# Kernel tuning notes

Hardware: AMD Instinct MI355X
Metric: run time of the kernel (lower is better)

The kernel has to match this reference:

```python
import jax, jax.numpy as jnp
import numpy as np

N = 500000   # num_nodes
B = 512      # batch_size
D = 128      # node_dim
G = 128      # global_dim
MC = 64      # max_cubes
M = 24       # max_moves_per_cube
H = 128      # MLP hidden
NEG = -1000000000.0


def setup_inputs() -> dict:
    key = jax.random.key(0)
    ks = jax.random.split(key, 8)
    node_features = jax.random.normal(ks[0], (N, D), jnp.float32)
    global_features = jax.random.normal(ks[1], (B, G), jnp.float32)
    cube_mask = jax.random.randint(ks[2], (N,), 0, 2) == 1
    batch = jnp.sort(jax.random.randint(ks[3], (N,), 0, B))
    move_mask = jax.random.randint(ks[4], (B, MC, M), 0, 2) == 1
    W1 = jax.random.normal(ks[5], (D + G, H), jnp.float32) * 0.05
    b1 = jnp.zeros((H,), jnp.float32)
    W2 = jax.random.normal(ks[6], (H, M), jnp.float32) * 0.05
    b2 = jnp.zeros((M,), jnp.float32)
    return {"node_features": node_features, "global_features": global_features,
            "W1": W1, "b1": b1, "W2": W2, "b2": b2,
            "cube_mask": cube_mask, "batch": batch, "move_mask": move_mask}


def reference(node_features, global_features, W1, b1, W2, b2, cube_mask, batch, move_mask):
    bsz = global_features.shape[0]
    max_cubes, moves = move_mask.shape[1], move_mask.shape[2]
    batch = batch.astype(jnp.int32)

    # gather global features per node, concat, small MLP (scores computed for all
    # nodes; only cube-node rows are ever scattered, matching the original math)
    combined = jnp.concatenate([node_features, global_features[batch]], axis=-1)  # [N, D+G]
    h = jax.nn.relu(combined @ W1 + b1)                                           # [N, H]
    scores = h @ W2 + b2                                                          # [N, M]

    # per-batch cumulative cube count (batch is sorted): cube_idx_in_batch
    mask_i = cube_mask.astype(jnp.int32)
    cum = jnp.cumsum(mask_i)                                   # inclusive prefix count of cubes
    counts = jax.ops.segment_sum(mask_i, batch, num_segments=bsz)
    offsets = jnp.concatenate([jnp.zeros((1,), jnp.int32),
                               jnp.cumsum(counts)[:-1].astype(jnp.int32)])
    cube_idx = cum - 1 - offsets[batch]                        # index of cube within its graph

    valid = cube_mask & (cube_idx < max_cubes)
    ib = jnp.where(valid, batch, bsz)      # out-of-range rows -> dropped
    ic = jnp.where(valid, cube_idx, 0)

    logits = jnp.full((bsz, max_cubes, moves), NEG, dtype=scores.dtype)
    logits = logits.at[ib, ic].set(scores, mode="drop")        # unique (ib, ic) per valid node

    logits_flat = logits.reshape(bsz, -1)
    logits_flat = jnp.where(move_mask.reshape(bsz, -1), logits_flat, NEG)
    return logits_flat
```

## Files before the change

kernel.cpp:

```cpp
#include <hip/hip_runtime.h>

typedef short bf16x8 __attribute__((ext_vector_type(8)));
typedef float f32x4 __attribute__((ext_vector_type(4)));

#define NEGV -1000000000.0f

__device__ __forceinline__ unsigned short f2bf(float f) {
    unsigned int u = __float_as_uint(f);
    u += 0x7FFFu + ((u >> 16) & 1u);
    return (unsigned short)(u >> 16);
}

__global__ void prep_kernel(const float* __restrict__ W1, const float* __restrict__ W2,
                            const int* __restrict__ batch, int N, int B,
                            int* __restrict__ batch_start,
                            unsigned short* __restrict__ w1t, unsigned short* __restrict__ w2t) {
    int idx = blockIdx.x * 256 + threadIdx.x;
    if (idx < N) {
        int bcur = batch[idx];
        if (idx == 0) {
            for (int bb = 0; bb <= bcur; ++bb) batch_start[bb] = 0;
        } else {
            int bprev = batch[idx - 1];
            for (int bb = bprev + 1; bb <= bcur; ++bb) batch_start[bb] = idx;
        }
        if (idx == N - 1) {
            for (int bb = bcur + 1; bb <= B; ++bb) batch_start[bb] = N;
        }
    }
    if (idx < 128 * 256) {
        int col = idx >> 8, k = idx & 255;
        w1t[col * 256 + k] = f2bf(W1[k * 128 + col]);
    }
    if (idx < 32 * 128) {
        int col = idx >> 7, k = idx & 127;
        w2t[col * 128 + k] = (col < 24) ? f2bf(W2[k * 24 + col]) : (unsigned short)0;
    }
}

__global__ void __launch_bounds__(256, 3)
fused_kernel(const float* __restrict__ nf, const float* __restrict__ gf,
             const unsigned short* __restrict__ w1t, const unsigned short* __restrict__ w2t,
             const float* __restrict__ b1, const float* __restrict__ b2,
             const int* __restrict__ cube_mask, const int* __restrict__ batch_start,
             const int* __restrict__ move_mask, float* __restrict__ out) {
    __shared__ __align__(16) char smemAB[(64 * 72 + 128 * 72) * 2];
    __shared__ __align__(16) unsigned short ldsW2[32][136];
    __shared__ int lds_node[64];
    __shared__ int wt[4];
    unsigned short (*ldsA)[72]  = (unsigned short (*)[72])smemAB;
    unsigned short (*ldsB)[72]  = (unsigned short (*)[72])(smemAB + 64 * 72 * 2);
    unsigned short (*ldsH)[136] = (unsigned short (*)[136])smemAB;

    int t = threadIdx.x;
    int blk = blockIdx.x;
    int lane = t & 63, w = t >> 6;

    int segs = batch_start[blk], sege = batch_start[blk + 1];

    if (t < 64) lds_node[t] = -1;

    {
        int col = t >> 3;
        int k0 = (t & 7) * 16;
        const unsigned short* src = w2t + col * 128 + k0;
        *(bf16x8*)&ldsW2[col][k0]     = *(const bf16x8*)(src);
        *(bf16x8*)&ldsW2[col][k0 + 8] = *(const bf16x8*)(src + 8);
    }
    int bcol = t >> 1, bh0 = (t & 1) * 32;
    bf16x8 fB[4];
    {
        const unsigned short* srcB = w1t + bcol * 256 + bh0;
        fB[0] = *(const bf16x8*)(srcB);      fB[1] = *(const bf16x8*)(srcB + 8);
        fB[2] = *(const bf16x8*)(srcB + 16); fB[3] = *(const bf16x8*)(srcB + 24);
    }
    int wm = w >> 1, wn = w & 1;
    float b1v[4];
#pragma unroll
    for (int nt = 0; nt < 4; ++nt) b1v[nt] = b1[wn * 64 + nt * 16 + (lane & 15)];
    float b2v[2];
    int mmv[8];
#pragma unroll
    for (int ct = 0; ct < 2; ++ct) {
        int m = ct * 16 + (lane & 15);
        if (m < 24) {
            b2v[ct] = b2[m];
#pragma unroll
            for (int rr = 0; rr < 4; ++rr) {
                int row = w * 16 + (lane >> 4) * 4 + rr;
                mmv[ct * 4 + rr] = move_mask[(size_t)(blk * 64 + row) * 24 + m];
            }
        } else {
            b2v[ct] = 0.f;
#pragma unroll
            for (int rr = 0; rr < 4; ++rr) mmv[ct * 4 + rr] = 0;
        }
    }
    __syncthreads();

    int found = 0;
    for (int pos = segs; pos < sege && found < 64; pos += 256) {
        int i = pos + t;
        int m = (i < sege) ? cube_mask[i] : 0;
        unsigned long long bal = __ballot(m != 0);
        int below = __popcll(bal & ((1ULL << lane) - 1ULL));
        if (lane == 0) wt[w] = __popcll(bal);
        __syncthreads();
        int waveOfs = 0, total = 0;
#pragma unroll
        for (int j = 0; j < 4; ++j) { int c = wt[j]; if (j < w) waveOfs += c; total += c; }
        int rank = found + waveOfs + below;
        if (m && rank < 64) lds_node[rank] = i;
        found += total;
        __syncthreads();
    }

    int r = t >> 2;
    int q = t & 3;
    int n = lds_node[r];
    int nrow = (n >= 0) ? n : 0;

    const float* srcN = nf + (size_t)nrow * 128 + q * 16;
    float4 fN[8];
#pragma unroll
    for (int i = 0; i < 4; ++i) {
        fN[i]     = *(const float4*)(srcN + i * 4);
        fN[4 + i] = *(const float4*)(srcN + 64 + i * 4);
    }

    f32x4 acc[2][4];
#pragma unroll
    for (int i = 0; i < 2; ++i)
#pragma unroll
        for (int j = 0; j < 4; ++j) acc[i][j] = (f32x4){0.f, 0.f, 0.f, 0.f};

    float4 fA[4];

#pragma unroll
    for (int c = 0; c < 4; ++c) {
        {
            float4 s0 = (c == 0) ? fN[0] : (c == 1) ? fN[4] : fA[0];
            float4 s1 = (c == 0) ? fN[1] : (c == 1) ? fN[5] : fA[1];
            float4 s2 = (c == 0) ? fN[2] : (c == 1) ? fN[6] : fA[2];
            float4 s3 = (c == 0) ? fN[3] : (c == 1) ? fN[7] : fA[3];
            unsigned short tmp[16];
            tmp[0]  = f2bf(s0.x); tmp[1]  = f2bf(s0.y); tmp[2]  = f2bf(s0.z); tmp[3]  = f2bf(s0.w);
            tmp[4]  = f2bf(s1.x); tmp[5]  = f2bf(s1.y); tmp[6]  = f2bf(s1.z); tmp[7]  = f2bf(s1.w);
            tmp[8]  = f2bf(s2.x); tmp[9]  = f2bf(s2.y); tmp[10] = f2bf(s2.z); tmp[11] = f2bf(s2.w);
            tmp[12] = f2bf(s3.x); tmp[13] = f2bf(s3.y); tmp[14] = f2bf(s3.z); tmp[15] = f2bf(s3.w);
            *(bf16x8*)&ldsA[r][q * 16]     = *(bf16x8*)&tmp[0];
            *(bf16x8*)&ldsA[r][q * 16 + 8] = *(bf16x8*)&tmp[8];
            *(bf16x8*)&ldsB[bcol][bh0]      = fB[0];
            *(bf16x8*)&ldsB[bcol][bh0 + 8]  = fB[1];
            *(bf16x8*)&ldsB[bcol][bh0 + 16] = fB[2];
            *(bf16x8*)&ldsB[bcol][bh0 + 24] = fB[3];
        }
        __syncthreads();
        if (c < 3) {
            const unsigned short* srcB = w1t + bcol * 256 + (c + 1) * 64 + bh0;
            fB[0] = *(const bf16x8*)(srcB);      fB[1] = *(const bf16x8*)(srcB + 8);
            fB[2] = *(const bf16x8*)(srcB + 16); fB[3] = *(const bf16x8*)(srcB + 24);
        }
        if (c == 1 || c == 2) {
            const float* srcG = gf + (size_t)blk * 128 + (c - 1) * 64 + q * 16;
            fA[0] = *(const float4*)(srcG);     fA[1] = *(const float4*)(srcG + 4);
            fA[2] = *(const float4*)(srcG + 8); fA[3] = *(const float4*)(srcG + 12);
        }
#pragma unroll
        for (int ks = 0; ks < 2; ++ks) {
            int ko = ks * 32 + (lane >> 4) * 8;
            bf16x8 af[2], bfr[4];
#pragma unroll
            for (int mt = 0; mt < 2; ++mt)
                af[mt] = *(const bf16x8*)&ldsA[wm * 32 + mt * 16 + (lane & 15)][ko];
#pragma unroll
            for (int nt = 0; nt < 4; ++nt)
                bfr[nt] = *(const bf16x8*)&ldsB[wn * 64 + nt * 16 + (lane & 15)][ko];
#pragma unroll
            for (int mt = 0; mt < 2; ++mt)
#pragma unroll
                for (int nt = 0; nt < 4; ++nt)
                    acc[mt][nt] = __builtin_amdgcn_mfma_f32_16x16x32_bf16(
                        af[mt], bfr[nt], acc[mt][nt], 0, 0, 0);
        }
        __syncthreads();
    }

#pragma unroll
    for (int nt = 0; nt < 4; ++nt) {
        int col = wn * 64 + nt * 16 + (lane & 15);
        float bias = b1v[nt];
#pragma unroll
        for (int mt = 0; mt < 2; ++mt) {
            int row0 = wm * 32 + mt * 16 + (lane >> 4) * 4;
#pragma unroll
            for (int rr = 0; rr < 4; ++rr) {
                float v = acc[mt][nt][rr] + bias;
                v = v > 0.f ? v : 0.f;
                ldsH[row0 + rr][col] = f2bf(v);
            }
        }
    }
    __syncthreads();

    f32x4 acc2[2];
    acc2[0] = (f32x4){0.f, 0.f, 0.f, 0.f};
    acc2[1] = (f32x4){0.f, 0.f, 0.f, 0.f};
#pragma unroll
    for (int ks = 0; ks < 4; ++ks) {
        int ko = ks * 32 + (lane >> 4) * 8;
        bf16x8 a2 = *(const bf16x8*)&ldsH[w * 16 + (lane & 15)][ko];
#pragma unroll
        for (int ct = 0; ct < 2; ++ct) {
            bf16x8 bw = *(const bf16x8*)&ldsW2[ct * 16 + (lane & 15)][ko];
            acc2[ct] = __builtin_amdgcn_mfma_f32_16x16x32_bf16(a2, bw, acc2[ct], 0, 0, 0);
        }
    }

#pragma unroll
    for (int ct = 0; ct < 2; ++ct) {
        int m = ct * 16 + (lane & 15);
        if (m >= 24) continue;
#pragma unroll
        for (int rr = 0; rr < 4; ++rr) {
            int row = w * 16 + (lane >> 4) * 4 + rr;
            size_t oidx = (size_t)(blk * 64 + row) * 24 + m;
            float v = acc2[ct][rr] + b2v[ct];
            bool keep = (lds_node[row] >= 0) && (mmv[ct * 4 + rr] != 0);
            out[oidx] = keep ? v : NEGV;
        }
    }
}

extern "C" void kernel_launch(void* const* d_in, const int* in_sizes, int n_in,
                              void* d_out, int out_size, void* d_ws, size_t ws_size,
                              hipStream_t stream) {
    const float* nf = (const float*)d_in[0];
    const float* gf = (const float*)d_in[1];
    const float* W1 = (const float*)d_in[2];
    const float* b1 = (const float*)d_in[3];
    const float* W2 = (const float*)d_in[4];
    const float* b2 = (const float*)d_in[5];
    const int* cube_mask = (const int*)d_in[6];
    const int* batch     = (const int*)d_in[7];
    const int* move_mask = (const int*)d_in[8];
    float* out = (float*)d_out;

    int N = in_sizes[6];
    int B = in_sizes[1] / 128;

    char* ws = (char*)d_ws;
    int* batch_start = (int*)(ws);
    unsigned short* w1t = (unsigned short*)(ws + 4096);
    unsigned short* w2t = (unsigned short*)(ws + 69632);

    int NB = (N + 255) / 256;
    prep_kernel<<<NB, 256, 0, stream>>>(W1, W2, batch, N, B, batch_start, w1t, w2t);
    fused_kernel<<<B, 256, 0, stream>>>(nf, gf, w1t, w2t, b1, b2,
                                        cube_mask, batch_start, move_mask, out);
    (void)n_in; (void)out_size; (void)ws_size;
}
```

Before: 17.86 us.

## Remove prep kernel; binary-search segments and convert W1/W2 in-block

Drops the separate prep kernel. Each block now finds its batch segment bounds by a 128-way parallel search over the sorted batch array, and converts W1/W2 from fp32 to bf16 into LDS itself. The GEMM chunk order is changed so the global-feature chunks run first while the search and node-feature loads are still in flight. This removes one launch and the 500k-element boundary pass, at the cost of every block redundantly reading and converting the fp32 weights and doing extra synchronised search rounds.

```diff
diff --git a/kernel.cpp b/kernel.cpp
--- a/kernel.cpp
+++ b/kernel.cpp
@@ -10,44 +10,22 @@
     u += 0x7FFFu + ((u >> 16) & 1u);
     return (unsigned short)(u >> 16);
 }
-
-__global__ void prep_kernel(const float* __restrict__ W1, const float* __restrict__ W2,
-                            const int* __restrict__ batch, int N, int B,
-                            int* __restrict__ batch_start,
-                            unsigned short* __restrict__ w1t, unsigned short* __restrict__ w2t) {
-    int idx = blockIdx.x * 256 + threadIdx.x;
-    if (idx < N) {
-        int bcur = batch[idx];
-        if (idx == 0) {
-            for (int bb = 0; bb <= bcur; ++bb) batch_start[bb] = 0;
-        } else {
-            int bprev = batch[idx - 1];
-            for (int bb = bprev + 1; bb <= bcur; ++bb) batch_start[bb] = idx;
-        }
-        if (idx == N - 1) {
-            for (int bb = bcur + 1; bb <= B; ++bb) batch_start[bb] = N;
-        }
-    }
-    if (idx < 128 * 256) {
-        int col = idx >> 8, k = idx & 255;
-        w1t[col * 256 + k] = f2bf(W1[k * 128 + col]);
-    }
-    if (idx < 32 * 128) {
-        int col = idx >> 7, k = idx & 127;
-        w2t[col * 128 + k] = (col < 24) ? f2bf(W2[k * 24 + col]) : (unsigned short)0;
-    }
+__device__ __forceinline__ unsigned int pack2(float a, float b) {
+    return (unsigned int)f2bf(a) | ((unsigned int)f2bf(b) << 16);
 }
 
 __global__ void __launch_bounds__(256, 3)
 fused_kernel(const float* __restrict__ nf, const float* __restrict__ gf,
-             const unsigned short* __restrict__ w1t, const unsigned short* __restrict__ w2t,
-             const float* __restrict__ b1, const float* __restrict__ b2,
-             const int* __restrict__ cube_mask, const int* __restrict__ batch_start,
-             const int* __restrict__ move_mask, float* __restrict__ out) {
+             const float* __restrict__ W1, const float* __restrict__ b1,
+             const float* __restrict__ W2, const float* __restrict__ b2,
+             const int* __restrict__ cube_mask, const int* __restrict__ batch,
+             const int* __restrict__ move_mask, float* __restrict__ out, int N) {
     __shared__ __align__(16) char smemAB[(64 * 72 + 128 * 72) * 2];
     __shared__ __align__(16) unsigned short ldsW2[32][136];
     __shared__ int lds_node[64];
     __shared__ int wt[4];
+    __shared__ unsigned long long swt[4];
+    __shared__ int seg[2];
     unsigned short (*ldsA)[72]  = (unsigned short (*)[72])smemAB;
     unsigned short (*ldsB)[72]  = (unsigned short (*)[72])(smemAB + 64 * 72 * 2);
     unsigned short (*ldsH)[136] = (unsigned short (*)[136])smemAB;
@@ -56,24 +34,14 @@
     int blk = blockIdx.x;
     int lane = t & 63, w = t >> 6;
 
-    int segs = batch_start[blk], sege = batch_start[blk + 1];
-
     if (t < 64) lds_node[t] = -1;
 
-    {
-        int col = t >> 3;
-        int k0 = (t & 7) * 16;
-        const unsigned short* src = w2t + col * 128 + k0;
-        *(bf16x8*)&ldsW2[col][k0]     = *(const bf16x8*)(src);
-        *(bf16x8*)&ldsW2[col][k0 + 8] = *(const bf16x8*)(src + 8);
-    }
-    int bcol = t >> 1, bh0 = (t & 1) * 32;
-    bf16x8 fB[4];
-    {
-        const unsigned short* srcB = w1t + bcol * 256 + bh0;
-        fB[0] = *(const bf16x8*)(srcB);      fB[1] = *(const bf16x8*)(srcB + 8);
-        fB[2] = *(const bf16x8*)(srcB + 16); fB[3] = *(const bf16x8*)(srcB + 24);
-    }
+    int w2col = t >> 3, w2k0 = (t & 7) * 16;
+    float w2v[16];
+#pragma unroll
+    for (int j = 0; j < 16; ++j)
+        w2v[j] = (w2col < 24) ? W2[(size_t)(w2k0 + j) * 24 + w2col] : 0.f;
+
     int wm = w >> 1, wn = w & 1;
     float b1v[4];
 #pragma unroll
@@ -96,7 +64,67 @@
             for (int rr = 0; rr < 4; ++rr) mmv[ct * 4 + rr] = 0;
         }
     }
-    __syncthreads();
+
+    int kp = t >> 3, hblk = t & 7;
+    float4 fW[8];
+    {
+        const float* s0 = W1 + (size_t)(128 + kp * 2) * 128 + hblk * 16;
+#pragma unroll
+        for (int i = 0; i < 4; ++i) {
+            fW[i]     = *(const float4*)(s0 + i * 4);
+            fW[4 + i] = *(const float4*)(s0 + 128 + i * 4);
+        }
+    }
+
+    int half = t >> 7, l = t & 127;
+    int target = blk + half;
+    int lo = -1, hi = N;
+#pragma unroll
+    for (int round = 0; round < 3; ++round) {
+        int span = hi - lo;
+        int pos = lo + (int)(((long long)span * (l + 1)) / 129);
+        int v = (pos >= 0) ? batch[pos] : -1;
+        unsigned long long bal = __ballot(v >= target);
+        if (lane == 0) swt[w] = bal;
+        __syncthreads();
+        unsigned long long mlow = swt[half * 2], mhigh = swt[half * 2 + 1];
+        int j0 = mlow ? __builtin_ctzll(mlow) : (mhigh ? 64 + __builtin_ctzll(mhigh) : -1);
+        if (j0 < 0) {
+            lo = lo + (int)(((long long)span * 128) / 129);
+        } else {
+            hi = lo + (int)(((long long)span * (j0 + 1)) / 129);
+            if (j0 > 0) lo = lo + (int)(((long long)span * j0) / 129);
+        }
+        __syncthreads();
+    }
+    if (l == 0) seg[half] = hi;
+
+#pragma unroll
+    for (int j = 0; j < 8; ++j)
+        *(unsigned int*)&ldsW2[w2col][w2k0 + 2 * j] = pack2(w2v[2 * j], w2v[2 * j + 1]);
+#pragma unroll
+    for (int j = 0; j < 16; ++j) {
+        float a  = ((const float*)&fW[j >> 2])[j & 3];
+        float bq = ((const float*)&fW[4 + (j >> 2)])[j & 3];
+        *(unsigned int*)&ldsB[hblk * 16 + j][kp * 2] = pack2(a, bq);
+    }
+    {
+        const float* s0 = W1 + (size_t)(192 + kp * 2) * 128 + hblk * 16;
+#pragma unroll
+        for (int i = 0; i < 4; ++i) {
+            fW[i]     = *(const float4*)(s0 + i * 4);
+            fW[4 + i] = *(const float4*)(s0 + 128 + i * 4);
+        }
+    }
+    int r = t >> 2, q = t & 3;
+    float4 fG[4];
+    {
+        const float* srcG = gf + (size_t)blk * 128 + q * 16;
+#pragma unroll
+        for (int i = 0; i < 4; ++i) fG[i] = *(const float4*)(srcG + i * 4);
+    }
+    __syncthreads();
+    int segs = seg[0], sege = seg[1];
 
     int found = 0;
     for (int pos = segs; pos < sege && found < 64; pos += 256) {
@@ -115,11 +143,8 @@
         __syncthreads();
     }
 
-    int r = t >> 2;
-    int q = t & 3;
     int n = lds_node[r];
     int nrow = (n >= 0) ? n : 0;
-
     const float* srcN = nf + (size_t)nrow * 128 + q * 16;
     float4 fN[8];
 #pragma unroll
@@ -134,57 +159,88 @@
 #pragma unroll
         for (int j = 0; j < 4; ++j) acc[i][j] = (f32x4){0.f, 0.f, 0.f, 0.f};
 
-    float4 fA[4];
-
-#pragma unroll
-    for (int c = 0; c < 4; ++c) {
-        {
-            float4 s0 = (c == 0) ? fN[0] : (c == 1) ? fN[4] : fA[0];
-            float4 s1 = (c == 0) ? fN[1] : (c == 1) ? fN[5] : fA[1];
-            float4 s2 = (c == 0) ? fN[2] : (c == 1) ? fN[6] : fA[2];
-            float4 s3 = (c == 0) ? fN[3] : (c == 1) ? fN[7] : fA[3];
-            unsigned short tmp[16];
-            tmp[0]  = f2bf(s0.x); tmp[1]  = f2bf(s0.y); tmp[2]  = f2bf(s0.z); tmp[3]  = f2bf(s0.w);
-            tmp[4]  = f2bf(s1.x); tmp[5]  = f2bf(s1.y); tmp[6]  = f2bf(s1.z); tmp[7]  = f2bf(s1.w);
-            tmp[8]  = f2bf(s2.x); tmp[9]  = f2bf(s2.y); tmp[10] = f2bf(s2.z); tmp[11] = f2bf(s2.w);
-            tmp[12] = f2bf(s3.x); tmp[13] = f2bf(s3.y); tmp[14] = f2bf(s3.z); tmp[15] = f2bf(s3.w);
-            *(bf16x8*)&ldsA[r][q * 16]     = *(bf16x8*)&tmp[0];
-            *(bf16x8*)&ldsA[r][q * 16 + 8] = *(bf16x8*)&tmp[8];
-            *(bf16x8*)&ldsB[bcol][bh0]      = fB[0];
-            *(bf16x8*)&ldsB[bcol][bh0 + 8]  = fB[1];
-            *(bf16x8*)&ldsB[bcol][bh0 + 16] = fB[2];
-            *(bf16x8*)&ldsB[bcol][bh0 + 24] = fB[3];
-        }
-        __syncthreads();
-        if (c < 3) {
-            const unsigned short* srcB = w1t + bcol * 256 + (c + 1) * 64 + bh0;
-            fB[0] = *(const bf16x8*)(srcB);      fB[1] = *(const bf16x8*)(srcB + 8);
-            fB[2] = *(const bf16x8*)(srcB + 16); fB[3] = *(const bf16x8*)(srcB + 24);
-        }
-        if (c == 1 || c == 2) {
-            const float* srcG = gf + (size_t)blk * 128 + (c - 1) * 64 + q * 16;
-            fA[0] = *(const float4*)(srcG);     fA[1] = *(const float4*)(srcG + 4);
-            fA[2] = *(const float4*)(srcG + 8); fA[3] = *(const float4*)(srcG + 12);
-        }
-#pragma unroll
-        for (int ks = 0; ks < 2; ++ks) {
-            int ko = ks * 32 + (lane >> 4) * 8;
-            bf16x8 af[2], bfr[4];
-#pragma unroll
-            for (int mt = 0; mt < 2; ++mt)
-                af[mt] = *(const bf16x8*)&ldsA[wm * 32 + mt * 16 + (lane & 15)][ko];
-#pragma unroll
-            for (int nt = 0; nt < 4; ++nt)
-                bfr[nt] = *(const bf16x8*)&ldsB[wn * 64 + nt * 16 + (lane & 15)][ko];
-#pragma unroll
-            for (int mt = 0; mt < 2; ++mt)
-#pragma unroll
-                for (int nt = 0; nt < 4; ++nt)
-                    acc[mt][nt] = __builtin_amdgcn_mfma_f32_16x16x32_bf16(
-                        af[mt], bfr[nt], acc[mt][nt], 0, 0, 0);
-        }
-        __syncthreads();
-    }
+#define STAGE_A(s0, s1, s2, s3) do {                                             \
+        unsigned short tmp[16];                                                  \
+        tmp[0]  = f2bf((s0).x); tmp[1]  = f2bf((s0).y); tmp[2]  = f2bf((s0).z); tmp[3]  = f2bf((s0).w); \
+        tmp[4]  = f2bf((s1).x); tmp[5]  = f2bf((s1).y); tmp[6]  = f2bf((s1).z); tmp[7]  = f2bf((s1).w); \
+        tmp[8]  = f2bf((s2).x); tmp[9]  = f2bf((s2).y); tmp[10] = f2bf((s2).z); tmp[11] = f2bf((s2).w); \
+        tmp[12] = f2bf((s3).x); tmp[13] = f2bf((s3).y); tmp[14] = f2bf((s3).z); tmp[15] = f2bf((s3).w); \
+        *(bf16x8*)&ldsA[r][q * 16]     = *(bf16x8*)&tmp[0];                      \
+        *(bf16x8*)&ldsA[r][q * 16 + 8] = *(bf16x8*)&tmp[8];                      \
+    } while (0)
+
+#define STAGE_B() do {                                                           \
+        _Pragma("unroll")                                                        \
+        for (int j = 0; j < 16; ++j) {                                           \
+            float a_  = ((const float*)&fW[j >> 2])[j & 3];                      \
+            float b_  = ((const float*)&fW[4 + (j >> 2)])[j & 3];                \
+            *(unsigned int*)&ldsB[hblk * 16 + j][kp * 2] = pack2(a_, b_);        \
+        }                                                                        \
+    } while (0)
+
+#define LOAD_W1(ch) do {                                                         \
+        const float* s0_ = W1 + (size_t)((ch) * 64 + kp * 2) * 128 + hblk * 16;  \
+        _Pragma("unroll")                                                        \
+        for (int i = 0; i < 4; ++i) {                                            \
+            fW[i]     = *(const float4*)(s0_ + i * 4);                           \
+            fW[4 + i] = *(const float4*)(s0_ + 128 + i * 4);                     \
+        }                                                                        \
+    } while (0)
+
+#define MFMA_CHUNK() do {                                                        \
+        _Pragma("unroll")                                                        \
+        for (int ks = 0; ks < 2; ++ks) {                                         \
+            int ko = ks * 32 + (lane >> 4) * 8;                                  \
+            bf16x8 af[2], bfr[4];                                                \
+            _Pragma("unroll")                                                    \
+            for (int mt = 0; mt < 2; ++mt)                                       \
+                af[mt] = *(const bf16x8*)&ldsA[wm * 32 + mt * 16 + (lane & 15)][ko]; \
+            _Pragma("unroll")                                                    \
+            for (int nt = 0; nt < 4; ++nt)                                       \
+                bfr[nt] = *(const bf16x8*)&ldsB[wn * 64 + nt * 16 + (lane & 15)][ko]; \
+            _Pragma("unroll")                                                    \
+            for (int mt = 0; mt < 2; ++mt)                                       \
+                _Pragma("unroll")                                                \
+                for (int nt = 0; nt < 4; ++nt)                                   \
+                    acc[mt][nt] = __builtin_amdgcn_mfma_f32_16x16x32_bf16(       \
+                        af[mt], bfr[nt], acc[mt][nt], 0, 0, 0);                  \
+        }                                                                        \
+    } while (0)
+
+    STAGE_A(fG[0], fG[1], fG[2], fG[3]);
+    __syncthreads();
+    {
+        const float* srcG = gf + (size_t)blk * 128 + 64 + q * 16;
+#pragma unroll
+        for (int i = 0; i < 4; ++i) fG[i] = *(const float4*)(srcG + i * 4);
+    }
+    MFMA_CHUNK();
+    __syncthreads();
+
+    STAGE_B();
+    LOAD_W1(0);
+    STAGE_A(fG[0], fG[1], fG[2], fG[3]);
+    __syncthreads();
+    MFMA_CHUNK();
+    __syncthreads();
+
+    STAGE_B();
+    LOAD_W1(1);
+    STAGE_A(fN[0], fN[1], fN[2], fN[3]);
+    __syncthreads();
+    MFMA_CHUNK();
+    __syncthreads();
+
+    STAGE_B();
+    STAGE_A(fN[4], fN[5], fN[6], fN[7]);
+    __syncthreads();
+    MFMA_CHUNK();
+    __syncthreads();
+
+#undef STAGE_A
+#undef STAGE_B
+#undef LOAD_W1
+#undef MFMA_CHUNK
 
 #pragma unroll
     for (int nt = 0; nt < 4; ++nt) {
@@ -249,14 +305,7 @@
     int N = in_sizes[6];
     int B = in_sizes[1] / 128;
 
-    char* ws = (char*)d_ws;
-    int* batch_start = (int*)(ws);
-    unsigned short* w1t = (unsigned short*)(ws + 4096);
-    unsigned short* w2t = (unsigned short*)(ws + 69632);
-
-    int NB = (N + 255) / 256;
-    prep_kernel<<<NB, 256, 0, stream>>>(W1, W2, batch, N, B, batch_start, w1t, w2t);
-    fused_kernel<<<B, 256, 0, stream>>>(nf, gf, w1t, w2t, b1, b2,
-                                        cube_mask, batch_start, move_mask, out);
-    (void)n_in; (void)out_size; (void)ws_size;
+    fused_kernel<<<B, 256, 0, stream>>>(nf, gf, W1, b1, W2, b2,
+                                        cube_mask, batch, move_mask, out, N);
+    (void)n_in; (void)out_size; (void)d_ws; (void)ws_size;
 }
```

Result: slower. 20.16 us (+12.9%).

## Overlap cube search with global-feature GEMM chunks using double-buffered LDS

Applied to the files above, without the earlier changes.

Reorders the first-layer GEMM so the two global-feature K-chunks are computed first, while the cube-mask scan and node-row gather are still in flight. The scan now reads a 1024-element window with one vectorised int4 load and a shuffle prefix sum, and only falls back to the ballot loop when that window does not hold 64 cubes. A and B tiles are double-buffered in LDS to remove one barrier per chunk. This doubles LDS use and lowers launch bounds to 2 blocks per CU, so fewer blocks can be resident.

```diff
diff --git a/kernel.cpp b/kernel.cpp
--- a/kernel.cpp
+++ b/kernel.cpp
@@ -38,43 +38,56 @@
     }
 }
 
-__global__ void __launch_bounds__(256, 3)
+__global__ void __launch_bounds__(256, 2)
 fused_kernel(const float* __restrict__ nf, const float* __restrict__ gf,
              const unsigned short* __restrict__ w1t, const unsigned short* __restrict__ w2t,
              const float* __restrict__ b1, const float* __restrict__ b2,
              const int* __restrict__ cube_mask, const int* __restrict__ batch_start,
-             const int* __restrict__ move_mask, float* __restrict__ out) {
-    __shared__ __align__(16) char smemAB[(64 * 72 + 128 * 72) * 2];
+             const int* __restrict__ move_mask, float* __restrict__ out, int N) {
+    __shared__ __align__(16) char smem[(64 * 72 + 128 * 72) * 2 * 2];
     __shared__ __align__(16) unsigned short ldsW2[32][136];
     __shared__ int lds_node[64];
     __shared__ int wt[4];
-    unsigned short (*ldsA)[72]  = (unsigned short (*)[72])smemAB;
-    unsigned short (*ldsB)[72]  = (unsigned short (*)[72])(smemAB + 64 * 72 * 2);
-    unsigned short (*ldsH)[136] = (unsigned short (*)[136])smemAB;
+    unsigned short (*ldsA0)[72]  = (unsigned short (*)[72])smem;
+    unsigned short (*ldsB0)[72]  = (unsigned short (*)[72])(smem + 9216);
+    unsigned short (*ldsA1)[72]  = (unsigned short (*)[72])(smem + 27648);
+    unsigned short (*ldsB1)[72]  = (unsigned short (*)[72])(smem + 27648 + 9216);
+    unsigned short (*ldsH)[136]  = (unsigned short (*)[136])smem;
 
     int t = threadIdx.x;
     int blk = blockIdx.x;
     int lane = t & 63, w = t >> 6;
+    int wm = w >> 1, wn = w & 1;
+    int r = t >> 2, q = t & 3;
+    int bcol = t >> 1, bh0 = (t & 1) * 32;
 
     int segs = batch_start[blk], sege = batch_start[blk + 1];
 
     if (t < 64) lds_node[t] = -1;
 
+    int w2col = t >> 3, w2k0 = (t & 7) * 16;
+    bf16x8 w2a, w2b;
     {
-        int col = t >> 3;
-        int k0 = (t & 7) * 16;
-        const unsigned short* src = w2t + col * 128 + k0;
-        *(bf16x8*)&ldsW2[col][k0]     = *(const bf16x8*)(src);
-        *(bf16x8*)&ldsW2[col][k0 + 8] = *(const bf16x8*)(src + 8);
-    }
-    int bcol = t >> 1, bh0 = (t & 1) * 32;
+        const unsigned short* src = w2t + w2col * 128 + w2k0;
+        w2a = *(const bf16x8*)(src);
+        w2b = *(const bf16x8*)(src + 8);
+    }
     bf16x8 fB[4];
+#define LOAD_W1(ch) do {                                                         \
+        const unsigned short* srcB = w1t + bcol * 256 + (ch) * 64 + bh0;         \
+        fB[0] = *(const bf16x8*)(srcB);      fB[1] = *(const bf16x8*)(srcB + 8); \
+        fB[2] = *(const bf16x8*)(srcB + 16); fB[3] = *(const bf16x8*)(srcB + 24);\
+    } while (0)
+    LOAD_W1(2);
+    float4 fGl[4], fGh[4];
     {
-        const unsigned short* srcB = w1t + bcol * 256 + bh0;
-        fB[0] = *(const bf16x8*)(srcB);      fB[1] = *(const bf16x8*)(srcB + 8);
-        fB[2] = *(const bf16x8*)(srcB + 16); fB[3] = *(const bf16x8*)(srcB + 24);
-    }
-    int wm = w >> 1, wn = w & 1;
+        const float* srcG = gf + (size_t)blk * 128 + q * 16;
+#pragma unroll
+        for (int i = 0; i < 4; ++i) {
+            fGl[i] = *(const float4*)(srcG + i * 4);
+            fGh[i] = *(const float4*)(srcG + 64 + i * 4);
+        }
+    }
     float b1v[4];
 #pragma unroll
     for (int nt = 0; nt < 4; ++nt) b1v[nt] = b1[wn * 64 + nt * 16 + (lane & 15)];
@@ -96,30 +109,117 @@
             for (int rr = 0; rr < 4; ++rr) mmv[ct * 4 + rr] = 0;
         }
     }
-    __syncthreads();
-
-    int found = 0;
-    for (int pos = segs; pos < sege && found < 64; pos += 256) {
+
+    int base = segs & ~3;
+    if (base > N - 1024) base = (N - 1024) & ~3;
+    int4 cmv = *(const int4*)(cube_mask + base + t * 4);
+
+#define STAGE_A(AB, s0, s1, s2, s3) do {                                         \
+        unsigned short tmp[16];                                                  \
+        tmp[0]  = f2bf((s0).x); tmp[1]  = f2bf((s0).y); tmp[2]  = f2bf((s0).z); tmp[3]  = f2bf((s0).w); \
+        tmp[4]  = f2bf((s1).x); tmp[5]  = f2bf((s1).y); tmp[6]  = f2bf((s1).z); tmp[7]  = f2bf((s1).w); \
+        tmp[8]  = f2bf((s2).x); tmp[9]  = f2bf((s2).y); tmp[10] = f2bf((s2).z); tmp[11] = f2bf((s2).w); \
+        tmp[12] = f2bf((s3).x); tmp[13] = f2bf((s3).y); tmp[14] = f2bf((s3).z); tmp[15] = f2bf((s3).w); \
+        *(bf16x8*)&AB[r][q * 16]     = *(bf16x8*)&tmp[0];                        \
+        *(bf16x8*)&AB[r][q * 16 + 8] = *(bf16x8*)&tmp[8];                        \
+    } while (0)
+#define STAGE_B(BB) do {                                                         \
+        *(bf16x8*)&BB[bcol][bh0]      = fB[0];                                   \
+        *(bf16x8*)&BB[bcol][bh0 + 8]  = fB[1];                                   \
+        *(bf16x8*)&BB[bcol][bh0 + 16] = fB[2];                                   \
+        *(bf16x8*)&BB[bcol][bh0 + 24] = fB[3];                                   \
+    } while (0)
+#define MFMA_CHUNK(AA, BB) do {                                                  \
+        _Pragma("unroll")                                                        \
+        for (int ks = 0; ks < 2; ++ks) {                                         \
+            int ko = ks * 32 + (lane >> 4) * 8;                                  \
+            bf16x8 af[2], bfr[4];                                                \
+            _Pragma("unroll")                                                    \
+            for (int mt = 0; mt < 2; ++mt)                                       \
+                af[mt] = *(const bf16x8*)&AA[wm * 32 + mt * 16 + (lane & 15)][ko]; \
+            _Pragma("unroll")                                                    \
+            for (int nt = 0; nt < 4; ++nt)                                       \
+                bfr[nt] = *(const bf16x8*)&BB[wn * 64 + nt * 16 + (lane & 15)][ko]; \
+            _Pragma("unroll")                                                    \
+            for (int mt = 0; mt < 2; ++mt)                                       \
+                _Pragma("unroll")                                                \
+                for (int nt = 0; nt < 4; ++nt)                                   \
+                    acc[mt][nt] = __builtin_amdgcn_mfma_f32_16x16x32_bf16(       \
+                        af[mt], bfr[nt], acc[mt][nt], 0, 0, 0);                  \
+        }                                                                        \
+    } while (0)
+
+    *(bf16x8*)&ldsW2[w2col][w2k0]     = w2a;
+    *(bf16x8*)&ldsW2[w2col][w2k0 + 8] = w2b;
+    STAGE_A(ldsA0, fGl[0], fGl[1], fGl[2], fGl[3]);
+    STAGE_B(ldsB0);
+    LOAD_W1(3);
+
+    f32x4 acc[2][4];
+#pragma unroll
+    for (int i = 0; i < 2; ++i)
+#pragma unroll
+        for (int j = 0; j < 4; ++j) acc[i][j] = (f32x4){0.f, 0.f, 0.f, 0.f};
+
+    __syncthreads();
+
+    STAGE_A(ldsA1, fGh[0], fGh[1], fGh[2], fGh[3]);
+    STAGE_B(ldsB1);
+    LOAD_W1(0);
+
+    int c_t = 0;
+#pragma unroll
+    for (int j = 0; j < 4; ++j) {
+        int i = base + t * 4 + j;
+        int mk = ((const int*)&cmv)[j];
+        c_t += (i >= segs && i < sege && mk != 0) ? 1 : 0;
+    }
+    int inc = c_t;
+#pragma unroll
+    for (int d = 1; d < 64; d <<= 1) {
+        int o = __shfl_up(inc, d);
+        if (lane >= d) inc += o;
+    }
+    if (lane == 63) wt[w] = inc;
+
+    MFMA_CHUNK(ldsA0, ldsB0);
+    __syncthreads();
+
+    int waveOfs = 0, total = 0;
+#pragma unroll
+    for (int j = 0; j < 4; ++j) { int c = wt[j]; if (j < w) waveOfs += c; total += c; }
+    {
+        int rank = waveOfs + (inc - c_t);
+#pragma unroll
+        for (int j = 0; j < 4; ++j) {
+            int i = base + t * 4 + j;
+            int mk = ((const int*)&cmv)[j];
+            if (i >= segs && i < sege && mk != 0) {
+                if (rank < 64) lds_node[rank] = i;
+                ++rank;
+            }
+        }
+    }
+    int found = total;
+    for (int pos = base + 1024; pos < sege && found < 64; pos += 256) {
         int i = pos + t;
-        int m = (i < sege) ? cube_mask[i] : 0;
-        unsigned long long bal = __ballot(m != 0);
+        int mk = (i < sege) ? cube_mask[i] : 0;
+        unsigned long long bal = __ballot(mk != 0);
         int below = __popcll(bal & ((1ULL << lane) - 1ULL));
+        __syncthreads();
         if (lane == 0) wt[w] = __popcll(bal);
         __syncthreads();
-        int waveOfs = 0, total = 0;
-#pragma unroll
-        for (int j = 0; j < 4; ++j) { int c = wt[j]; if (j < w) waveOfs += c; total += c; }
-        int rank = found + waveOfs + below;
-        if (m && rank < 64) lds_node[rank] = i;
-        found += total;
-        __syncthreads();
-    }
-
-    int r = t >> 2;
-    int q = t & 3;
+        int wofs = 0, tot = 0;
+#pragma unroll
+        for (int j = 0; j < 4; ++j) { int c = wt[j]; if (j < w) wofs += c; tot += c; }
+        int rk = found + wofs + below;
+        if (mk && rk < 64) lds_node[rk] = i;
+        found += tot;
+    }
+    __syncthreads();
+
     int n = lds_node[r];
     int nrow = (n >= 0) ? n : 0;
-
     const float* srcN = nf + (size_t)nrow * 128 + q * 16;
     float4 fN[8];
 #pragma unroll
@@ -128,63 +228,23 @@
         fN[4 + i] = *(const float4*)(srcN + 64 + i * 4);
     }
 
-    f32x4 acc[2][4];
-#pragma unroll
-    for (int i = 0; i < 2; ++i)
-#pragma unroll
-        for (int j = 0; j < 4; ++j) acc[i][j] = (f32x4){0.f, 0.f, 0.f, 0.f};
-
-    float4 fA[4];
-
-#pragma unroll
-    for (int c = 0; c < 4; ++c) {
-        {
-            float4 s0 = (c == 0) ? fN[0] : (c == 1) ? fN[4] : fA[0];
-            float4 s1 = (c == 0) ? fN[1] : (c == 1) ? fN[5] : fA[1];
-            float4 s2 = (c == 0) ? fN[2] : (c == 1) ? fN[6] : fA[2];
-            float4 s3 = (c == 0) ? fN[3] : (c == 1) ? fN[7] : fA[3];
-            unsigned short tmp[16];
-            tmp[0]  = f2bf(s0.x); tmp[1]  = f2bf(s0.y); tmp[2]  = f2bf(s0.z); tmp[3]  = f2bf(s0.w);
-            tmp[4]  = f2bf(s1.x); tmp[5]  = f2bf(s1.y); tmp[6]  = f2bf(s1.z); tmp[7]  = f2bf(s1.w);
-            tmp[8]  = f2bf(s2.x); tmp[9]  = f2bf(s2.y); tmp[10] = f2bf(s2.z); tmp[11] = f2bf(s2.w);
-            tmp[12] = f2bf(s3.x); tmp[13] = f2bf(s3.y); tmp[14] = f2bf(s3.z); tmp[15] = f2bf(s3.w);
-            *(bf16x8*)&ldsA[r][q * 16]     = *(bf16x8*)&tmp[0];
-            *(bf16x8*)&ldsA[r][q * 16 + 8] = *(bf16x8*)&tmp[8];
-            *(bf16x8*)&ldsB[bcol][bh0]      = fB[0];
-            *(bf16x8*)&ldsB[bcol][bh0 + 8]  = fB[1];
-            *(bf16x8*)&ldsB[bcol][bh0 + 16] = fB[2];
-            *(bf16x8*)&ldsB[bcol][bh0 + 24] = fB[3];
-        }
-        __syncthreads();
-        if (c < 3) {
-            const unsigned short* srcB = w1t + bcol * 256 + (c + 1) * 64 + bh0;
-            fB[0] = *(const bf16x8*)(srcB);      fB[1] = *(const bf16x8*)(srcB + 8);
-            fB[2] = *(const bf16x8*)(srcB + 16); fB[3] = *(const bf16x8*)(srcB + 24);
-        }
-        if (c == 1 || c == 2) {
-            const float* srcG = gf + (size_t)blk * 128 + (c - 1) * 64 + q * 16;
-            fA[0] = *(const float4*)(srcG);     fA[1] = *(const float4*)(srcG + 4);
-            fA[2] = *(const float4*)(srcG + 8); fA[3] = *(const float4*)(srcG + 12);
-        }
-#pragma unroll
-        for (int ks = 0; ks < 2; ++ks) {
-            int ko = ks * 32 + (lane >> 4) * 8;
-            bf16x8 af[2], bfr[4];
-#pragma unroll
-            for (int mt = 0; mt < 2; ++mt)
-                af[mt] = *(const bf16x8*)&ldsA[wm * 32 + mt * 16 + (lane & 15)][ko];
-#pragma unroll
-            for (int nt = 0; nt < 4; ++nt)
-                bfr[nt] = *(const bf16x8*)&ldsB[wn * 64 + nt * 16 + (lane & 15)][ko];
-#pragma unroll
-            for (int mt = 0; mt < 2; ++mt)
-#pragma unroll
-                for (int nt = 0; nt < 4; ++nt)
-                    acc[mt][nt] = __builtin_amdgcn_mfma_f32_16x16x32_bf16(
-                        af[mt], bfr[nt], acc[mt][nt], 0, 0, 0);
-        }
-        __syncthreads();
-    }
+    MFMA_CHUNK(ldsA1, ldsB1);
+    STAGE_B(ldsB0);
+    LOAD_W1(1);
+    STAGE_A(ldsA0, fN[0], fN[1], fN[2], fN[3]);
+    __syncthreads();
+
+    MFMA_CHUNK(ldsA0, ldsB0);
+    STAGE_A(ldsA1, fN[4], fN[5], fN[6], fN[7]);
+    STAGE_B(ldsB1);
+    __syncthreads();
+
+    MFMA_CHUNK(ldsA1, ldsB1);
+
+#undef STAGE_A
+#undef STAGE_B
+#undef LOAD_W1
+#undef MFMA_CHUNK
 
 #pragma unroll
     for (int nt = 0; nt < 4; ++nt) {
@@ -257,6 +317,6 @@
     int NB = (N + 255) / 256;
     prep_kernel<<<NB, 256, 0, stream>>>(W1, W2, batch, N, B, batch_start, w1t, w2t);
     fused_kernel<<<B, 256, 0, stream>>>(nf, gf, w1t, w2t, b1, b2,
-                                        cube_mask, batch_start, move_mask, out);
+                                        cube_mask, batch_start, move_mask, out, N);
     (void)n_in; (void)out_size; (void)ws_size;
 }
```

Result: slower. 18.40 us (+3.0%).
